# Kernel tuning notes

Hardware: AMD Instinct MI355X
Metric: run time of the kernel (lower is better)

Reference implementation:

```python
import jax, jax.numpy as jnp
import numpy as np

N_NODES = 50000
N_EDGES = 600000
IN_DIM = 128
OUT_DIM = 128
EPS = 1e-12  # guards sqrt grad at exactly-zero diffs (matches torch.norm subgradient behavior)


def setup_inputs() -> dict:
    key = jax.random.key(0)
    k1, k2, k3, k4, k5 = jax.random.split(key, 5)
    h = jax.random.normal(k1, (N_NODES, IN_DIM), dtype=jnp.float32)
    # xavier-uniform-ish scale for fc weight [out_dim, in_dim]
    lim = float(np.sqrt(6.0 / (IN_DIM + OUT_DIM)))
    W_fc = jax.random.uniform(k2, (OUT_DIM, IN_DIM), dtype=jnp.float32, minval=-lim, maxval=lim)
    beta = jax.random.uniform(k3, (1,), dtype=jnp.float32)  # Tensor(1).uniform_(0,1)
    src = jax.random.randint(k4, (N_EDGES,), 0, N_NODES, dtype=jnp.int32)
    dst = jax.random.randint(k5, (N_EDGES,), 0, N_NODES, dtype=jnp.int32)
    return {"h": h, "W_fc": W_fc, "beta": beta, "src": src, "dst": dst}


def reference(h, W_fc, beta, src, dst):
    n = h.shape[0]
    # z = fc(h)  (dropout omitted for determinism; see notes)
    z = h @ W_fc.T  # [N, out_dim]
    zs = z[src]     # [E, out_dim] gather
    zd = z[dst]     # [E, out_dim] gather
    # RBF edge attention: e = -beta * ||z_src - z_dst||_2
    sq = jnp.sum((zs - zd) ** 2, axis=1)          # [E]
    e = -beta[0] * jnp.sqrt(sq + EPS)             # [E]
    # segment softmax over incoming edges of each dst node
    m = jax.ops.segment_max(e, dst, num_segments=n)   # [N], -inf for empty
    ex = jnp.exp(e - m[dst])                          # [E]
    denom = jax.ops.segment_sum(ex, dst, num_segments=n)  # [N]
    alpha = ex / denom[dst]                           # [E]
    # scatter-weighted sum of src features into dst nodes
    h_out = jax.ops.segment_sum(alpha[:, None] * zs, dst, num_segments=n)  # [N, out_dim]
    return h_out
```

## Files before the change

kernel.cpp:

```cpp
#include <hip/hip_runtime.h>
#include <math.h>

#define N_NODES 50000
#define N_EDGES 600000
#define DIM 128
#define BCAP 64

typedef __attribute__((ext_vector_type(8))) short bf16x8;
typedef __attribute__((ext_vector_type(4))) float f32x4;

static __device__ __forceinline__ short f2bf(float f) {
    unsigned u = __float_as_uint(f);
    unsigned r = (u + 0x7FFFu + ((u >> 16) & 1u)) >> 16;
    return (short)r;
}

#define UNPK(w, d0, d1)                         \
    d0 = __uint_as_float((w) << 16);            \
    d1 = __uint_as_float((w) & 0xFFFF0000u);

#define DPPADD(x, ctrl)                                                          \
    x += __int_as_float(__builtin_amdgcn_mov_dpp(__float_as_int(x), ctrl,        \
                                                 0xF, 0xF, true));
static __device__ __forceinline__ float row_sum16(float x) {
    DPPADD(x, 0xB1)
    DPPADD(x, 0x4E)
    DPPADD(x, 0x141)
    DPPADD(x, 0x140)
    return x;
}

__global__ __launch_bounds__(256) void prep_kernel(const float* __restrict__ W,
                                                   unsigned short* __restrict__ Wb,
                                                   int* __restrict__ cur,
                                                   int* __restrict__ cnt) {
    int gid = blockIdx.x * 256 + threadIdx.x;
    if (gid < N_NODES) {
        cur[gid] = 0;
        cnt[gid] = 0;
    }
    if (gid < DIM * DIM) Wb[gid] = (unsigned short)f2bf(W[gid]);
}

__global__ __launch_bounds__(256) void bfill_kernel(const int* __restrict__ src,
                                                    const int* __restrict__ dst,
                                                    int* __restrict__ cur,
                                                    int* __restrict__ lst) {
    int i = blockIdx.x * 256 + threadIdx.x;
    if (i >= N_EDGES) return;
    int d = dst[i];
    int pos = atomicAdd(cur + d, 1);
    if (pos < BCAP) lst[d * BCAP + pos] = src[i];
}

__global__ __launch_bounds__(256) void count_kernel(const int* __restrict__ dst,
                                                    int* __restrict__ cnt) {
    int i = blockIdx.x * 256 + threadIdx.x;
    if (i < N_EDGES) atomicAdd(cnt + dst[i], 1);
}

__global__ __launch_bounds__(256) void scan_a(const int* __restrict__ cnt,
                                              int* __restrict__ incl,
                                              int* __restrict__ bsum) {
    __shared__ int s[256];
    int i = blockIdx.x * 256 + threadIdx.x;
    s[threadIdx.x] = (i < N_NODES) ? cnt[i] : 0;
    __syncthreads();
    #pragma unroll
    for (int off = 1; off < 256; off <<= 1) {
        int t = (threadIdx.x >= off) ? s[threadIdx.x - off] : 0;
        __syncthreads();
        s[threadIdx.x] += t;
        __syncthreads();
    }
    if (i < N_NODES) incl[i] = s[threadIdx.x];
    if (threadIdx.x == 255) bsum[blockIdx.x] = s[255];
}

__global__ __launch_bounds__(256) void scan_b(int* __restrict__ bsum, int nb) {
    __shared__ int s[256];
    s[threadIdx.x] = (threadIdx.x < nb) ? bsum[threadIdx.x] : 0;
    __syncthreads();
    #pragma unroll
    for (int off = 1; off < 256; off <<= 1) {
        int t = (threadIdx.x >= off) ? s[threadIdx.x - off] : 0;
        __syncthreads();
        s[threadIdx.x] += t;
        __syncthreads();
    }
    if (threadIdx.x < nb) bsum[threadIdx.x] = s[threadIdx.x];
}

__global__ __launch_bounds__(256) void scan_c(int* __restrict__ incl_off,
                                              const int* __restrict__ cnt,
                                              const int* __restrict__ bsum) {
    int i = blockIdx.x * 256 + threadIdx.x;
    if (i >= N_NODES) return;
    int base = (blockIdx.x > 0) ? bsum[blockIdx.x - 1] : 0;
    incl_off[i] = incl_off[i] - cnt[i] + base;
}

__global__ __launch_bounds__(256) void cfill_kernel(const int* __restrict__ src,
                                                    const int* __restrict__ dst,
                                                    const int* __restrict__ off,
                                                    int* __restrict__ cur,
                                                    int* __restrict__ lst) {
    int i = blockIdx.x * 256 + threadIdx.x;
    if (i >= N_EDGES) return;
    int d = dst[i];
    int pos = atomicAdd(cur + d, 1);
    lst[off[d] + pos] = src[i];
}

__global__ __launch_bounds__(256) void gemm_kernel(const float* __restrict__ h,
                                                   const unsigned short* __restrict__ Wb,
                                                   unsigned short* __restrict__ zb) {
    int wave = blockIdx.x * 4 + (threadIdx.x >> 6);
    if (wave >= N_NODES / 16) return;
    int lane = threadIdx.x & 63;
    int lo = lane & 15;
    int hi = lane >> 4;
    long row0 = (long)wave * 16;

    bf16x8 afrag[4];
    const float* arow = h + (row0 + lo) * DIM;
    #pragma unroll
    for (int kt = 0; kt < 4; ++kt) {
        const float* ap = arow + kt * 32 + hi * 8;
        float4 f0 = *(const float4*)ap;
        float4 f1 = *(const float4*)(ap + 4);
        bf16x8 a;
        a[0] = f2bf(f0.x); a[1] = f2bf(f0.y); a[2] = f2bf(f0.z); a[3] = f2bf(f0.w);
        a[4] = f2bf(f1.x); a[5] = f2bf(f1.y); a[6] = f2bf(f1.z); a[7] = f2bf(f1.w);
        afrag[kt] = a;
    }

    #pragma unroll
    for (int ct = 0; ct < 8; ++ct) {
        f32x4 acc = {0.f, 0.f, 0.f, 0.f};
        const unsigned short* brow = Wb + (ct * 16 + lo) * DIM + hi * 8;
        #pragma unroll
        for (int kt = 0; kt < 4; ++kt) {
            bf16x8 b = *(const bf16x8*)(brow + kt * 32);
            acc = __builtin_amdgcn_mfma_f32_16x16x32_bf16(afrag[kt], b, acc, 0, 0, 0);
        }
        unsigned short* zp = zb + (row0 + hi * 4) * DIM + ct * 16 + lo;
        zp[0 * DIM] = (unsigned short)f2bf(acc[0]);
        zp[1 * DIM] = (unsigned short)f2bf(acc[1]);
        zp[2 * DIM] = (unsigned short)f2bf(acc[2]);
        zp[3 * DIM] = (unsigned short)f2bf(acc[3]);
    }
}

__global__ __launch_bounds__(256) void node_kernel(const unsigned short* __restrict__ zb,
                                                   const int* __restrict__ lst,
                                                   const int* __restrict__ off,
                                                   const int* __restrict__ degp,
                                                   int stride,
                                                   const float* __restrict__ beta,
                                                   float* __restrict__ out) {
    int node = blockIdx.x * 4 + (threadIdx.x >> 6);
    if (node >= N_NODES) return;
    int lane = threadIdx.x & 63;
    int q = lane >> 4;
    int ql = lane & 15;
    int deg = degp[node];
    int start;
    if (stride > 0) {
        if (deg > BCAP) deg = BCAP;
        start = node * stride;
    } else {
        start = off[node];
    }
    float nbet = -beta[0];

    uint4 zdw = *(const uint4*)(zb + (long)node * DIM + ql * 8);
    float zd[8];
    UNPK(zdw.x, zd[0], zd[1]) UNPK(zdw.y, zd[2], zd[3])
    UNPK(zdw.z, zd[4], zd[5]) UNPK(zdw.w, zd[6], zd[7])

    float sden = 0.0f;
    float acc[8];
    #pragma unroll
    for (int i = 0; i < 8; ++i) acc[i] = 0.0f;

    for (int cb = 0; cb < deg; cb += 64) {
        int nch = deg - cb;
        if (nch > 64) nch = 64;
        int sj = (lane < nch) ? lst[start + cb + lane] : 0;

        for (int jb = 0; jb < nch; jb += 8) {
            int jo0 = jb + q;
            int jo1 = jb + 4 + q;
            bool v0 = jo0 < nch;
            bool v1 = jo1 < nch;
            int s0 = __shfl(sj, v0 ? jo0 : 0, 64);
            int s1 = __shfl(sj, v1 ? jo1 : 0, 64);
            uint4 aw0 = *(const uint4*)(zb + (long)s0 * DIM + ql * 8);
            uint4 aw1 = *(const uint4*)(zb + (long)s1 * DIM + ql * 8);
            float a0[8], a1[8];
            UNPK(aw0.x, a0[0], a0[1]) UNPK(aw0.y, a0[2], a0[3])
            UNPK(aw0.z, a0[4], a0[5]) UNPK(aw0.w, a0[6], a0[7])
            UNPK(aw1.x, a1[0], a1[1]) UNPK(aw1.y, a1[2], a1[3])
            UNPK(aw1.z, a1[4], a1[5]) UNPK(aw1.w, a1[6], a1[7])

            float p0 = 0.0f, p1 = 0.0f;
            #pragma unroll
            for (int i = 0; i < 8; ++i) {
                float d0 = a0[i] - zd[i];
                p0 += d0 * d0;
                float d1 = a1[i] - zd[i];
                p1 += d1 * d1;
            }
            p0 = row_sum16(p0);
            p1 = row_sum16(p1);
            float w0 = v0 ? __expf(nbet * __builtin_amdgcn_sqrtf(p0 + 1e-12f)) : 0.0f;
            float w1 = v1 ? __expf(nbet * __builtin_amdgcn_sqrtf(p1 + 1e-12f)) : 0.0f;
            sden += w0 + w1;
            #pragma unroll
            for (int i = 0; i < 8; ++i) acc[i] += w0 * a0[i] + w1 * a1[i];
        }
    }

    #define CMB(v) v += __shfl_xor(v, 16, 64); v += __shfl_xor(v, 32, 64);
    CMB(sden)
    CMB(acc[0]) CMB(acc[1]) CMB(acc[2]) CMB(acc[3])
    CMB(acc[4]) CMB(acc[5]) CMB(acc[6]) CMB(acc[7])
    #undef CMB

    float inv = (deg > 0) ? 1.0f / sden : 0.0f;
    if (q == 0) {
        float* orow = out + (long)node * DIM + ql * 8;
        *(float4*)orow =
            make_float4(acc[0] * inv, acc[1] * inv, acc[2] * inv, acc[3] * inv);
        *(float4*)(orow + 4) =
            make_float4(acc[4] * inv, acc[5] * inv, acc[6] * inv, acc[7] * inv);
    }
}

extern "C" void kernel_launch(void* const* d_in, const int* in_sizes, int n_in,
                              void* d_out, int out_size, void* d_ws, size_t ws_size,
                              hipStream_t stream) {
    const float* h    = (const float*)d_in[0];
    const float* W    = (const float*)d_in[1];
    const float* beta = (const float*)d_in[2];
    const int* src    = (const int*)d_in[3];
    const int* dst    = (const int*)d_in[4];
    float* out = (float*)d_out;

    const size_t bucket_total = (3200000ull + 3200000 + 150000 + 256 + 8192) * 4;
    const bool use_bucket = ws_size >= bucket_total;
    const size_t lst_len = use_bucket ? 3200000 : 600000;

    float* ws  = (float*)d_ws;
    unsigned short* zb = (unsigned short*)ws;
    int* lst   = (int*)(ws + 3200000);
    int* cnt   = (int*)(ws + 3200000 + lst_len);
    int* cur   = cnt + 50000;
    int* off   = cur + 50000;
    int* bsum  = off + 50000;
    unsigned short* Wb = (unsigned short*)(bsum + 256);

    const int gemm_blocks = (N_NODES / 16 + 3) / 4;

    prep_kernel<<<196, 256, 0, stream>>>(W, Wb, cur, cnt);
    if (use_bucket) {
        bfill_kernel<<<(N_EDGES + 255) / 256, 256, 0, stream>>>(src, dst, cur, lst);
        gemm_kernel<<<gemm_blocks, 256, 0, stream>>>(h, Wb, zb);
        node_kernel<<<N_NODES / 4, 256, 0, stream>>>(zb, lst, cur , cur, BCAP,
                                                     beta, out);
    } else {
        count_kernel<<<(N_EDGES + 255) / 256, 256, 0, stream>>>(dst, cnt);
        scan_a<<<196, 256, 0, stream>>>(cnt, off, bsum);
        scan_b<<<1, 256, 0, stream>>>(bsum, 196);
        scan_c<<<196, 256, 0, stream>>>(off, cnt, bsum);
        cfill_kernel<<<(N_EDGES + 255) / 256, 256, 0, stream>>>(src, dst, off, cur, lst);
        gemm_kernel<<<gemm_blocks, 256, 0, stream>>>(h, Wb, zb);
        node_kernel<<<N_NODES / 4, 256, 0, stream>>>(zb, lst, off, cnt, 0, beta, out);
    }
}
```

Before: 161.6 us.

## Fuse bucket fill into GEMM kernel, widen node gather batch, use hardware bf16 convert

Merges the edge bucket-fill pass into the GEMM launch with a grid-stride loop, removing one kernel launch and letting the atomic fill overlap with the MFMA work. The node kernel now issues four neighbour row loads per iteration instead of two, exposing more memory-level parallelism for the gathers at some cost in registers. Software bf16 rounding is replaced with the v_cvt_pk_bf16_f32 instruction. In the new gather loop the shuffle index is no longer clamped for invalid lanes; those lanes still get zero weight, but they may read rows for stale list entries.

```diff
diff --git a/kernel.cpp b/kernel.cpp
--- a/kernel.cpp
+++ b/kernel.cpp
@@ -9,10 +9,13 @@
 typedef __attribute__((ext_vector_type(8))) short bf16x8;
 typedef __attribute__((ext_vector_type(4))) float f32x4;
 
-static __device__ __forceinline__ short f2bf(float f) {
-    unsigned u = __float_as_uint(f);
-    unsigned r = (u + 0x7FFFu + ((u >> 16) & 1u)) >> 16;
-    return (short)r;
+static __device__ __forceinline__ unsigned cvt_pk_bf16(float a, float b) {
+    unsigned r;
+    asm("v_cvt_pk_bf16_f32 %0, %1, %2" : "=v"(r) : "v"(a), "v"(b));
+    return r;
+}
+static __device__ __forceinline__ unsigned short f2bf(float f) {
+    return (unsigned short)cvt_pk_bf16(f, f);
 }
 
 #define UNPK(w, d0, d1)                         \
@@ -39,18 +42,72 @@
         cur[gid] = 0;
         cnt[gid] = 0;
     }
-    if (gid < DIM * DIM) Wb[gid] = (unsigned short)f2bf(W[gid]);
-}
-
-__global__ __launch_bounds__(256) void bfill_kernel(const int* __restrict__ src,
-                                                    const int* __restrict__ dst,
-                                                    int* __restrict__ cur,
-                                                    int* __restrict__ lst) {
-    int i = blockIdx.x * 256 + threadIdx.x;
-    if (i >= N_EDGES) return;
-    int d = dst[i];
-    int pos = atomicAdd(cur + d, 1);
-    if (pos < BCAP) lst[d * BCAP + pos] = src[i];
+    if (gid < DIM * DIM) Wb[gid] = f2bf(W[gid]);
+}
+
+static __device__ __forceinline__ void gemm_body(const float* __restrict__ h,
+                                                 const unsigned short* __restrict__ Wb,
+                                                 unsigned short* __restrict__ zb) {
+    int wave = blockIdx.x * 4 + (threadIdx.x >> 6);
+    if (wave >= N_NODES / 16) return;
+    int lane = threadIdx.x & 63;
+    int lo = lane & 15;
+    int hi = lane >> 4;
+    long row0 = (long)wave * 16;
+
+    bf16x8 afrag[4];
+    const float* arow = h + (row0 + lo) * DIM;
+    #pragma unroll
+    for (int kt = 0; kt < 4; ++kt) {
+        const float* ap = arow + kt * 32 + hi * 8;
+        float4 f0 = *(const float4*)ap;
+        float4 f1 = *(const float4*)(ap + 4);
+        union { unsigned u[4]; bf16x8 v; } c;
+        c.u[0] = cvt_pk_bf16(f0.x, f0.y);
+        c.u[1] = cvt_pk_bf16(f0.z, f0.w);
+        c.u[2] = cvt_pk_bf16(f1.x, f1.y);
+        c.u[3] = cvt_pk_bf16(f1.z, f1.w);
+        afrag[kt] = c.v;
+    }
+
+    #pragma unroll
+    for (int ct = 0; ct < 8; ++ct) {
+        f32x4 acc = {0.f, 0.f, 0.f, 0.f};
+        const unsigned short* brow = Wb + (ct * 16 + lo) * DIM + hi * 8;
+        #pragma unroll
+        for (int kt = 0; kt < 4; ++kt) {
+            bf16x8 b = *(const bf16x8*)(brow + kt * 32);
+            acc = __builtin_amdgcn_mfma_f32_16x16x32_bf16(afrag[kt], b, acc, 0, 0, 0);
+        }
+        unsigned short* zp = zb + (row0 + hi * 4) * DIM + ct * 16 + lo;
+        zp[0 * DIM] = f2bf(acc[0]);
+        zp[1 * DIM] = f2bf(acc[1]);
+        zp[2 * DIM] = f2bf(acc[2]);
+        zp[3 * DIM] = f2bf(acc[3]);
+    }
+}
+
+__global__ __launch_bounds__(256) void gemm_fill_kernel(const float* __restrict__ h,
+                                                        const unsigned short* __restrict__ Wb,
+                                                        unsigned short* __restrict__ zb,
+                                                        const int* __restrict__ src,
+                                                        const int* __restrict__ dst,
+                                                        int* __restrict__ cur,
+                                                        int* __restrict__ lst) {
+    int gid = blockIdx.x * 256 + threadIdx.x;
+    int nth = gridDim.x * 256;
+    for (int i = gid; i < N_EDGES; i += nth) {
+        int d = dst[i];
+        int pos = atomicAdd(cur + d, 1);
+        if (pos < BCAP) lst[d * BCAP + pos] = src[i];
+    }
+    gemm_body(h, Wb, zb);
+}
+
+__global__ __launch_bounds__(256) void gemm_kernel(const float* __restrict__ h,
+                                                   const unsigned short* __restrict__ Wb,
+                                                   unsigned short* __restrict__ zb) {
+    gemm_body(h, Wb, zb);
 }
 
 __global__ __launch_bounds__(256) void count_kernel(const int* __restrict__ dst,
@@ -110,46 +167,6 @@
     int d = dst[i];
     int pos = atomicAdd(cur + d, 1);
     lst[off[d] + pos] = src[i];
-}
-
-__global__ __launch_bounds__(256) void gemm_kernel(const float* __restrict__ h,
-                                                   const unsigned short* __restrict__ Wb,
-                                                   unsigned short* __restrict__ zb) {
-    int wave = blockIdx.x * 4 + (threadIdx.x >> 6);
-    if (wave >= N_NODES / 16) return;
-    int lane = threadIdx.x & 63;
-    int lo = lane & 15;
-    int hi = lane >> 4;
-    long row0 = (long)wave * 16;
-
-    bf16x8 afrag[4];
-    const float* arow = h + (row0 + lo) * DIM;
-    #pragma unroll
-    for (int kt = 0; kt < 4; ++kt) {
-        const float* ap = arow + kt * 32 + hi * 8;
-        float4 f0 = *(const float4*)ap;
-        float4 f1 = *(const float4*)(ap + 4);
-        bf16x8 a;
-        a[0] = f2bf(f0.x); a[1] = f2bf(f0.y); a[2] = f2bf(f0.z); a[3] = f2bf(f0.w);
-        a[4] = f2bf(f1.x); a[5] = f2bf(f1.y); a[6] = f2bf(f1.z); a[7] = f2bf(f1.w);
-        afrag[kt] = a;
-    }
-
-    #pragma unroll
-    for (int ct = 0; ct < 8; ++ct) {
-        f32x4 acc = {0.f, 0.f, 0.f, 0.f};
-        const unsigned short* brow = Wb + (ct * 16 + lo) * DIM + hi * 8;
-        #pragma unroll
-        for (int kt = 0; kt < 4; ++kt) {
-            bf16x8 b = *(const bf16x8*)(brow + kt * 32);
-            acc = __builtin_amdgcn_mfma_f32_16x16x32_bf16(afrag[kt], b, acc, 0, 0, 0);
-        }
-        unsigned short* zp = zb + (row0 + hi * 4) * DIM + ct * 16 + lo;
-        zp[0 * DIM] = (unsigned short)f2bf(acc[0]);
-        zp[1 * DIM] = (unsigned short)f2bf(acc[1]);
-        zp[2 * DIM] = (unsigned short)f2bf(acc[2]);
-        zp[3 * DIM] = (unsigned short)f2bf(acc[3]);
-    }
 }
 
 __global__ __launch_bounds__(256) void node_kernel(const unsigned short* __restrict__ zb,
@@ -189,36 +206,39 @@
         if (nch > 64) nch = 64;
         int sj = (lane < nch) ? lst[start + cb + lane] : 0;
 
-        for (int jb = 0; jb < nch; jb += 8) {
-            int jo0 = jb + q;
-            int jo1 = jb + 4 + q;
-            bool v0 = jo0 < nch;
-            bool v1 = jo1 < nch;
-            int s0 = __shfl(sj, v0 ? jo0 : 0, 64);
-            int s1 = __shfl(sj, v1 ? jo1 : 0, 64);
-            uint4 aw0 = *(const uint4*)(zb + (long)s0 * DIM + ql * 8);
-            uint4 aw1 = *(const uint4*)(zb + (long)s1 * DIM + ql * 8);
-            float a0[8], a1[8];
-            UNPK(aw0.x, a0[0], a0[1]) UNPK(aw0.y, a0[2], a0[3])
-            UNPK(aw0.z, a0[4], a0[5]) UNPK(aw0.w, a0[6], a0[7])
-            UNPK(aw1.x, a1[0], a1[1]) UNPK(aw1.y, a1[2], a1[3])
-            UNPK(aw1.z, a1[4], a1[5]) UNPK(aw1.w, a1[6], a1[7])
-
-            float p0 = 0.0f, p1 = 0.0f;
+        for (int jb = 0; jb < nch; jb += 16) {
+            int sv[4];
+            bool vv[4];
             #pragma unroll
-            for (int i = 0; i < 8; ++i) {
-                float d0 = a0[i] - zd[i];
-                p0 += d0 * d0;
-                float d1 = a1[i] - zd[i];
-                p1 += d1 * d1;
+            for (int k = 0; k < 4; ++k) {
+                int jo = jb + k * 4 + q;
+                sv[k] = __shfl(sj, jo, 64);
+                vv[k] = jo < nch;
             }
-            p0 = row_sum16(p0);
-            p1 = row_sum16(p1);
-            float w0 = v0 ? __expf(nbet * __builtin_amdgcn_sqrtf(p0 + 1e-12f)) : 0.0f;
-            float w1 = v1 ? __expf(nbet * __builtin_amdgcn_sqrtf(p1 + 1e-12f)) : 0.0f;
-            sden += w0 + w1;
+            uint4 aw[4];
             #pragma unroll
-            for (int i = 0; i < 8; ++i) acc[i] += w0 * a0[i] + w1 * a1[i];
+            for (int k = 0; k < 4; ++k)
+                aw[k] = *(const uint4*)(zb + (long)sv[k] * DIM + ql * 8);
+
+            #pragma unroll
+            for (int k = 0; k < 4; ++k) {
+                float a[8];
+                UNPK(aw[k].x, a[0], a[1]) UNPK(aw[k].y, a[2], a[3])
+                UNPK(aw[k].z, a[4], a[5]) UNPK(aw[k].w, a[6], a[7])
+                float p = 0.0f;
+                #pragma unroll
+                for (int i = 0; i < 8; ++i) {
+                    float d = a[i] - zd[i];
+                    p += d * d;
+                }
+                p = row_sum16(p);
+                float w = vv[k]
+                        ? __expf(nbet * __builtin_amdgcn_sqrtf(p + 1e-12f))
+                        : 0.0f;
+                sden += w;
+                #pragma unroll
+                for (int i = 0; i < 8; ++i) acc[i] += w * a[i];
+            }
         }
     }
 
@@ -265,8 +285,7 @@
 
     prep_kernel<<<196, 256, 0, stream>>>(W, Wb, cur, cnt);
     if (use_bucket) {
-        bfill_kernel<<<(N_EDGES + 255) / 256, 256, 0, stream>>>(src, dst, cur, lst);
-        gemm_kernel<<<gemm_blocks, 256, 0, stream>>>(h, Wb, zb);
+        gemm_fill_kernel<<<gemm_blocks, 256, 0, stream>>>(h, Wb, zb, src, dst, cur, lst);
         node_kernel<<<N_NODES / 4, 256, 0, stream>>>(zb, lst, cur , cur, BCAP,
                                                      beta, out);
     } else {
```

Measured after the change: 166.2 us. 1.03x slower.

## Fuse bucket fill with GEMM in one interleaved launch and use packed bf16 converts

Applied to the files above, without the earlier changes.

Merges the edge-bucket fill kernel and the node-feature GEMM into one launch. Every fourth block runs the GEMM and the other three run edge bucketing, so the atomic-heavy fill and the MFMA work overlap on the GPU and one kernel launch is saved. It also swaps the manual round-to-nearest bf16 conversion for the v_cvt_pk_bf16_f32 instruction, which packs two values per instruction. The interleaving puts different workloads side by side in one grid and adds a dependence on inline asm.

```diff
diff --git a/kernel.cpp b/kernel.cpp
--- a/kernel.cpp
+++ b/kernel.cpp
@@ -9,10 +9,13 @@
 typedef __attribute__((ext_vector_type(8))) short bf16x8;
 typedef __attribute__((ext_vector_type(4))) float f32x4;
 
-static __device__ __forceinline__ short f2bf(float f) {
-    unsigned u = __float_as_uint(f);
-    unsigned r = (u + 0x7FFFu + ((u >> 16) & 1u)) >> 16;
-    return (short)r;
+static __device__ __forceinline__ unsigned cvt_pk_bf16(float a, float b) {
+    unsigned r;
+    asm("v_cvt_pk_bf16_f32 %0, %1, %2" : "=v"(r) : "v"(a), "v"(b));
+    return r;
+}
+static __device__ __forceinline__ unsigned short f2bf(float f) {
+    return (unsigned short)cvt_pk_bf16(f, f);
 }
 
 #define UNPK(w, d0, d1)                         \
@@ -39,18 +42,78 @@
         cur[gid] = 0;
         cnt[gid] = 0;
     }
-    if (gid < DIM * DIM) Wb[gid] = (unsigned short)f2bf(W[gid]);
-}
-
-__global__ __launch_bounds__(256) void bfill_kernel(const int* __restrict__ src,
-                                                    const int* __restrict__ dst,
-                                                    int* __restrict__ cur,
-                                                    int* __restrict__ lst) {
-    int i = blockIdx.x * 256 + threadIdx.x;
-    if (i >= N_EDGES) return;
-    int d = dst[i];
-    int pos = atomicAdd(cur + d, 1);
-    if (pos < BCAP) lst[d * BCAP + pos] = src[i];
+    if (gid < DIM * DIM) Wb[gid] = f2bf(W[gid]);
+}
+
+static __device__ __forceinline__ void gemm_body(const float* __restrict__ h,
+                                                 const unsigned short* __restrict__ Wb,
+                                                 unsigned short* __restrict__ zb,
+                                                 int wave, int lane) {
+    int lo = lane & 15;
+    int hi = lane >> 4;
+    long row0 = (long)wave * 16;
+
+    bf16x8 afrag[4];
+    const float* arow = h + (row0 + lo) * DIM;
+    #pragma unroll
+    for (int kt = 0; kt < 4; ++kt) {
+        const float* ap = arow + kt * 32 + hi * 8;
+        float4 f0 = *(const float4*)ap;
+        float4 f1 = *(const float4*)(ap + 4);
+        union { unsigned u[4]; bf16x8 v; } c;
+        c.u[0] = cvt_pk_bf16(f0.x, f0.y);
+        c.u[1] = cvt_pk_bf16(f0.z, f0.w);
+        c.u[2] = cvt_pk_bf16(f1.x, f1.y);
+        c.u[3] = cvt_pk_bf16(f1.z, f1.w);
+        afrag[kt] = c.v;
+    }
+
+    #pragma unroll
+    for (int ct = 0; ct < 8; ++ct) {
+        f32x4 acc = {0.f, 0.f, 0.f, 0.f};
+        const unsigned short* brow = Wb + (ct * 16 + lo) * DIM + hi * 8;
+        #pragma unroll
+        for (int kt = 0; kt < 4; ++kt) {
+            bf16x8 b = *(const bf16x8*)(brow + kt * 32);
+            acc = __builtin_amdgcn_mfma_f32_16x16x32_bf16(afrag[kt], b, acc, 0, 0, 0);
+        }
+        unsigned short* zp = zb + (row0 + hi * 4) * DIM + ct * 16 + lo;
+        zp[0 * DIM] = f2bf(acc[0]);
+        zp[1 * DIM] = f2bf(acc[1]);
+        zp[2 * DIM] = f2bf(acc[2]);
+        zp[3 * DIM] = f2bf(acc[3]);
+    }
+}
+
+__global__ __launch_bounds__(256) void fg_kernel(const float* __restrict__ h,
+                                                 const unsigned short* __restrict__ Wb,
+                                                 unsigned short* __restrict__ zb,
+                                                 const int* __restrict__ src,
+                                                 const int* __restrict__ dst,
+                                                 int* __restrict__ cur,
+                                                 int* __restrict__ lst) {
+    int bid = blockIdx.x;
+    if (bid & 3) {
+        int f = (bid >> 2) * 3 + (bid & 3) - 1;
+        int i = f * 256 + threadIdx.x;
+        if (i < N_EDGES) {
+            int d = dst[i];
+            int pos = atomicAdd(cur + d, 1);
+            if (pos < BCAP) lst[d * BCAP + pos] = src[i];
+        }
+        return;
+    }
+    int wave = (bid >> 2) * 4 + (threadIdx.x >> 6);
+    if (wave >= N_NODES / 16) return;
+    gemm_body(h, Wb, zb, wave, threadIdx.x & 63);
+}
+
+__global__ __launch_bounds__(256) void gemm_kernel(const float* __restrict__ h,
+                                                   const unsigned short* __restrict__ Wb,
+                                                   unsigned short* __restrict__ zb) {
+    int wave = blockIdx.x * 4 + (threadIdx.x >> 6);
+    if (wave >= N_NODES / 16) return;
+    gemm_body(h, Wb, zb, wave, threadIdx.x & 63);
 }
 
 __global__ __launch_bounds__(256) void count_kernel(const int* __restrict__ dst,
@@ -110,46 +173,6 @@
     int d = dst[i];
     int pos = atomicAdd(cur + d, 1);
     lst[off[d] + pos] = src[i];
-}
-
-__global__ __launch_bounds__(256) void gemm_kernel(const float* __restrict__ h,
-                                                   const unsigned short* __restrict__ Wb,
-                                                   unsigned short* __restrict__ zb) {
-    int wave = blockIdx.x * 4 + (threadIdx.x >> 6);
-    if (wave >= N_NODES / 16) return;
-    int lane = threadIdx.x & 63;
-    int lo = lane & 15;
-    int hi = lane >> 4;
-    long row0 = (long)wave * 16;
-
-    bf16x8 afrag[4];
-    const float* arow = h + (row0 + lo) * DIM;
-    #pragma unroll
-    for (int kt = 0; kt < 4; ++kt) {
-        const float* ap = arow + kt * 32 + hi * 8;
-        float4 f0 = *(const float4*)ap;
-        float4 f1 = *(const float4*)(ap + 4);
-        bf16x8 a;
-        a[0] = f2bf(f0.x); a[1] = f2bf(f0.y); a[2] = f2bf(f0.z); a[3] = f2bf(f0.w);
-        a[4] = f2bf(f1.x); a[5] = f2bf(f1.y); a[6] = f2bf(f1.z); a[7] = f2bf(f1.w);
-        afrag[kt] = a;
-    }
-
-    #pragma unroll
-    for (int ct = 0; ct < 8; ++ct) {
-        f32x4 acc = {0.f, 0.f, 0.f, 0.f};
-        const unsigned short* brow = Wb + (ct * 16 + lo) * DIM + hi * 8;
-        #pragma unroll
-        for (int kt = 0; kt < 4; ++kt) {
-            bf16x8 b = *(const bf16x8*)(brow + kt * 32);
-            acc = __builtin_amdgcn_mfma_f32_16x16x32_bf16(afrag[kt], b, acc, 0, 0, 0);
-        }
-        unsigned short* zp = zb + (row0 + hi * 4) * DIM + ct * 16 + lo;
-        zp[0 * DIM] = (unsigned short)f2bf(acc[0]);
-        zp[1 * DIM] = (unsigned short)f2bf(acc[1]);
-        zp[2 * DIM] = (unsigned short)f2bf(acc[2]);
-        zp[3 * DIM] = (unsigned short)f2bf(acc[3]);
-    }
 }
 
 __global__ __launch_bounds__(256) void node_kernel(const unsigned short* __restrict__ zb,
@@ -261,12 +284,9 @@
     int* bsum  = off + 50000;
     unsigned short* Wb = (unsigned short*)(bsum + 256);
 
-    const int gemm_blocks = (N_NODES / 16 + 3) / 4;
-
     prep_kernel<<<196, 256, 0, stream>>>(W, Wb, cur, cnt);
     if (use_bucket) {
-        bfill_kernel<<<(N_EDGES + 255) / 256, 256, 0, stream>>>(src, dst, cur, lst);
-        gemm_kernel<<<gemm_blocks, 256, 0, stream>>>(h, Wb, zb);
+        fg_kernel<<<3126, 256, 0, stream>>>(h, Wb, zb, src, dst, cur, lst);
         node_kernel<<<N_NODES / 4, 256, 0, stream>>>(zb, lst, cur , cur, BCAP,
                                                      beta, out);
     } else {
@@ -275,7 +295,7 @@
         scan_b<<<1, 256, 0, stream>>>(bsum, 196);
         scan_c<<<196, 256, 0, stream>>>(off, cnt, bsum);
         cfill_kernel<<<(N_EDGES + 255) / 256, 256, 0, stream>>>(src, dst, off, cur, lst);
-        gemm_kernel<<<gemm_blocks, 256, 0, stream>>>(h, Wb, zb);
+        gemm_kernel<<<(N_NODES / 16 + 3) / 4, 256, 0, stream>>>(h, Wb, zb);
         node_kernel<<<N_NODES / 4, 256, 0, stream>>>(zb, lst, off, cnt, 0, beta, out);
     }
 }
```

Measured after the change: 170.8 us. 5.7% more time.
